# Kernel tuning notes

Measured on AMD Instinct MI355X. Metric: run time of the kernel, lower is better.

## Reference

```python
import jax, jax.numpy as jnp
import numpy as np

N = 1024
X_DIM = 128
Y_DIM = 128
HIDDEN = 256


def setup_inputs() -> dict:
    key = jax.random.key(0)
    ks = jax.random.split(key, 6)
    x_samples = jax.random.normal(ks[0], (N, X_DIM), dtype=jnp.float32)
    y_samples = jax.random.normal(ks[1], (N, Y_DIM), dtype=jnp.float32)
    in_dim = X_DIM + Y_DIM
    # Linear params (kaiming-uniform-ish small init)
    W1 = jax.random.normal(ks[2], (in_dim, HIDDEN), dtype=jnp.float32) / np.sqrt(in_dim)
    b1 = jnp.zeros((HIDDEN,), dtype=jnp.float32)
    W2 = jax.random.normal(ks[3], (HIDDEN, 1), dtype=jnp.float32) / np.sqrt(HIDDEN)
    b2 = jnp.zeros((1,), dtype=jnp.float32)
    return {"x_samples": x_samples, "y_samples": y_samples,
            "W1": W1, "b1": b1, "W2": W2, "b2": b2}


def reference(x_samples, y_samples, W1, b1, W2, b2):
    n = y_samples.shape[0]
    W1x, W1y = W1[:X_DIM], W1[X_DIM:]
    xp = x_samples @ W1x          # [N, H]  (x_tile[i, j] = x[j])
    yp = y_samples @ W1y          # [N, H]  (y_tile[i, j] = y[i])
    # T0: F(cat([x_i, y_i])) on the diagonal pairs -> [N, 1]
    T0 = jax.nn.relu(xp + yp + b1) @ W2 + b2
    # T1: F over all pairs (i, j) -> [N, N, 1]
    h = jax.nn.relu(yp[:, None, :] + xp[None, :, :] + b1)   # [N, N, H]
    T1 = h @ W2 + b2                                        # [N, N, 1]
    lse = jax.scipy.special.logsumexp(T1, axis=1)           # [N, 1] over dim=1
    lower_bound = T0.mean() - (lse.mean() - jnp.log(jnp.float32(n)))
    return lower_bound
```

## Files before the change

kernel.cpp:

```cpp
#include <hip/hip_runtime.h>

#define N_SAMP 1024
#define XD     128
#define HID    256


__global__ __launch_bounds__(256) void gemm_xy(
    const float* __restrict__ x, const float* __restrict__ y,
    const float* __restrict__ W1, const float* __restrict__ b1,
    float* __restrict__ xpbT, float* __restrict__ ypT,
    float* __restrict__ S, float* __restrict__ T0sum)
{
    const int k  = threadIdx.x;
    const int r0 = blockIdx.x * 4;

    if (threadIdx.x < 4) S[blockIdx.x * 4 + threadIdx.x] = 0.f;
    if (blockIdx.x == 0 && threadIdx.x == 4) T0sum[0] = 0.f;

    float ax0 = 0.f, ax1 = 0.f, ax2 = 0.f, ax3 = 0.f;
    float ay0 = 0.f, ay1 = 0.f, ay2 = 0.f, ay3 = 0.f;

    #pragma unroll 4
    for (int d = 0; d < XD; ++d) {
        const float wx = W1[d * HID + k];
        const float wy = W1[(XD + d) * HID + k];
        ax0 = fmaf(x[(r0 + 0) * XD + d], wx, ax0);
        ax1 = fmaf(x[(r0 + 1) * XD + d], wx, ax1);
        ax2 = fmaf(x[(r0 + 2) * XD + d], wx, ax2);
        ax3 = fmaf(x[(r0 + 3) * XD + d], wx, ax3);
        ay0 = fmaf(y[(r0 + 0) * XD + d], wy, ay0);
        ay1 = fmaf(y[(r0 + 1) * XD + d], wy, ay1);
        ay2 = fmaf(y[(r0 + 2) * XD + d], wy, ay2);
        ay3 = fmaf(y[(r0 + 3) * XD + d], wy, ay3);
    }

    const float bk = b1[k];
    float4 xs = make_float4(ax0 + bk, ax1 + bk, ax2 + bk, ax3 + bk);
    float4 ys = make_float4(ay0, ay1, ay2, ay3);
    *(float4*)&xpbT[k * N_SAMP + r0] = xs;
    *(float4*)&ypT [k * N_SAMP + r0] = ys;
}

__global__ __launch_bounds__(256) void pair_lse(
    const float* __restrict__ ypT, const float* __restrict__ xpbT,
    const float* __restrict__ W2,
    float* __restrict__ S, float* __restrict__ T0sum)
{
    const int tid = threadIdx.x;
    const int tj  = tid & 15;
    const int ti  = tid >> 4;
    const int bj  = blockIdx.x;
    const int bi  = blockIdx.y;
    const int j0  = bj * 64 + tj * 4;
    const int i0  = bi * 32 + ti * 2;

    float acc[2][4];
    #pragma unroll
    for (int a = 0; a < 2; ++a)
        #pragma unroll
        for (int b = 0; b < 4; ++b) acc[a][b] = 0.f;

    #pragma unroll 4
    for (int k = 0; k < HID; ++k) {
        const float4 xv = *(const float4*)&xpbT[k * N_SAMP + j0];
        const float2 yv = *(const float2*)&ypT [k * N_SAMP + i0];
        const float  w  = W2[k];
        acc[0][0] = fmaf(fmaxf(yv.x + xv.x, 0.f), w, acc[0][0]);
        acc[0][1] = fmaf(fmaxf(yv.x + xv.y, 0.f), w, acc[0][1]);
        acc[0][2] = fmaf(fmaxf(yv.x + xv.z, 0.f), w, acc[0][2]);
        acc[0][3] = fmaf(fmaxf(yv.x + xv.w, 0.f), w, acc[0][3]);
        acc[1][0] = fmaf(fmaxf(yv.y + xv.x, 0.f), w, acc[1][0]);
        acc[1][1] = fmaf(fmaxf(yv.y + xv.y, 0.f), w, acc[1][1]);
        acc[1][2] = fmaf(fmaxf(yv.y + xv.z, 0.f), w, acc[1][2]);
        acc[1][3] = fmaf(fmaxf(yv.y + xv.w, 0.f), w, acc[1][3]);
    }

    #pragma unroll
    for (int a = 0; a < 2; ++a) {
        float e = __expf(acc[a][0]) + __expf(acc[a][1])
                + __expf(acc[a][2]) + __expf(acc[a][3]);
        #pragma unroll
        for (int off = 8; off; off >>= 1) e += __shfl_xor(e, off, 16);
        if (tj == 0) atomicAdd(&S[i0 + a], e);
    }

    if (bj == (bi >> 1)) {
        float dv = 0.f;
        #pragma unroll
        for (int a = 0; a < 2; ++a)
            #pragma unroll
            for (int b = 0; b < 4; ++b)
                if (i0 + a == j0 + b) dv += acc[a][b];
        #pragma unroll
        for (int off = 32; off; off >>= 1) dv += __shfl_xor(dv, off, 64);
        if ((tid & 63) == 0) atomicAdd(T0sum, dv);
    }
}

__global__ __launch_bounds__(256) void finalize(
    const float* __restrict__ S, const float* __restrict__ T0sum,
    const float* __restrict__ b2, float* __restrict__ out)
{
    __shared__ float red[4];
    const int tid = threadIdx.x;

    float ls = 0.f;
    for (int i = tid; i < N_SAMP; i += 256) ls += logf(S[i]);
    #pragma unroll
    for (int off = 32; off; off >>= 1) ls += __shfl_xor(ls, off, 64);
    if ((tid & 63) == 0) red[tid >> 6] = ls;
    __syncthreads();

    if (tid == 0) {
        const float lse_sum = red[0] + red[1] + red[2] + red[3];
        const float t0_mean  = T0sum[0] / (float)N_SAMP + b2[0];
        const float lse_mean = lse_sum / (float)N_SAMP + b2[0] - logf((float)N_SAMP);
        out[0] = t0_mean - lse_mean;
    }
}

extern "C" void kernel_launch(void* const* d_in, const int* in_sizes, int n_in,
                              void* d_out, int out_size, void* d_ws, size_t ws_size,
                              hipStream_t stream)
{
    const float* x  = (const float*)d_in[0];
    const float* y  = (const float*)d_in[1];
    const float* W1 = (const float*)d_in[2];
    const float* b1 = (const float*)d_in[3];
    const float* W2 = (const float*)d_in[4];
    const float* b2 = (const float*)d_in[5];

    float* ws   = (float*)d_ws;
    float* S    = ws;
    float* T0s  = ws + 1024;
    float* xpbT = ws + 2048;
    float* ypT  = ws + 2048 + HID * N_SAMP;

    gemm_xy <<<dim3(N_SAMP / 4), dim3(256), 0, stream>>>(x, y, W1, b1,
                                                         xpbT, ypT, S, T0s);
    pair_lse<<<dim3(16, 32),     dim3(256), 0, stream>>>(ypT, xpbT, W2, S, T0s);
    finalize<<<dim3(1),          dim3(256), 0, stream>>>(S, T0s, b2, (float*)d_out);
}
```

Measured before the change: 114.4 us.

## Stage y tile in LDS and compute 4x4 pair outputs per thread

```diff
diff --git a/kernel.cpp b/kernel.cpp
--- a/kernel.cpp
+++ b/kernel.cpp
@@ -41,42 +41,55 @@
     *(float4*)&ypT [k * N_SAMP + r0] = ys;
 }
 
-__global__ __launch_bounds__(256) void pair_lse(
+__global__ __launch_bounds__(128) void pair_lse(
     const float* __restrict__ ypT, const float* __restrict__ xpbT,
     const float* __restrict__ W2,
     float* __restrict__ S, float* __restrict__ T0sum)
 {
+    __shared__ float yl[HID * 32];
+
     const int tid = threadIdx.x;
     const int tj  = tid & 15;
     const int ti  = tid >> 4;
-    const int bj  = blockIdx.x;
-    const int bi  = blockIdx.y;
-    const int j0  = bj * 64 + tj * 4;
-    const int i0  = bi * 32 + ti * 2;
+    const int jb  = blockIdx.x * 64;
+    const int ib  = blockIdx.y * 32;
+    const int j0  = jb + tj * 4;
+    const int i0  = ib + ti * 4;
 
-    float acc[2][4];
     #pragma unroll
-    for (int a = 0; a < 2; ++a)
+    for (int s = 0; s < 16; ++s) {
+        const int f  = s * 128 + tid;
+        const int k  = f >> 3;
+        const int iq = (f & 7) * 4;
+        *(float4*)&yl[k * 32 + iq] =
+            *(const float4*)&ypT[k * N_SAMP + ib + iq];
+    }
+    __syncthreads();
+
+    float acc[4][4];
+    #pragma unroll
+    for (int a = 0; a < 4; ++a)
         #pragma unroll
         for (int b = 0; b < 4; ++b) acc[a][b] = 0.f;
 
-    #pragma unroll 4
+    const int ti4 = ti * 4;
+
+    #pragma unroll 8
     for (int k = 0; k < HID; ++k) {
         const float4 xv = *(const float4*)&xpbT[k * N_SAMP + j0];
-        const float2 yv = *(const float2*)&ypT [k * N_SAMP + i0];
+        const float4 yv = *(const float4*)&yl[k * 32 + ti4];
         const float  w  = W2[k];
-        acc[0][0] = fmaf(fmaxf(yv.x + xv.x, 0.f), w, acc[0][0]);
-        acc[0][1] = fmaf(fmaxf(yv.x + xv.y, 0.f), w, acc[0][1]);
-        acc[0][2] = fmaf(fmaxf(yv.x + xv.z, 0.f), w, acc[0][2]);
-        acc[0][3] = fmaf(fmaxf(yv.x + xv.w, 0.f), w, acc[0][3]);
-        acc[1][0] = fmaf(fmaxf(yv.y + xv.x, 0.f), w, acc[1][0]);
-        acc[1][1] = fmaf(fmaxf(yv.y + xv.y, 0.f), w, acc[1][1]);
-        acc[1][2] = fmaf(fmaxf(yv.y + xv.z, 0.f), w, acc[1][2]);
-        acc[1][3] = fmaf(fmaxf(yv.y + xv.w, 0.f), w, acc[1][3]);
+        const float xs[4] = {xv.x, xv.y, xv.z, xv.w};
+        const float ys[4] = {yv.x, yv.y, yv.z, yv.w};
+        #pragma unroll
+        for (int a = 0; a < 4; ++a)
+            #pragma unroll
+            for (int b = 0; b < 4; ++b)
+                acc[a][b] = fmaf(fmaxf(ys[a] + xs[b], 0.f), w, acc[a][b]);
     }
 
     #pragma unroll
-    for (int a = 0; a < 2; ++a) {
+    for (int a = 0; a < 4; ++a) {
         float e = __expf(acc[a][0]) + __expf(acc[a][1])
                 + __expf(acc[a][2]) + __expf(acc[a][3]);
         #pragma unroll
@@ -84,13 +97,18 @@
         if (tj == 0) atomicAdd(&S[i0 + a], e);
     }
 
-    if (bj == (bi >> 1)) {
+    if ((int)blockIdx.x == (int)(blockIdx.y >> 1)) {
         float dv = 0.f;
         #pragma unroll
-        for (int a = 0; a < 2; ++a)
-            #pragma unroll
-            for (int b = 0; b < 4; ++b)
-                if (i0 + a == j0 + b) dv += acc[a][b];
+        for (int a = 0; a < 4; ++a) {
+            const int dd = i0 + a - j0;
+            float t = 0.f;
+            if      (dd == 0) t = acc[a][0];
+            else if (dd == 1) t = acc[a][1];
+            else if (dd == 2) t = acc[a][2];
+            else if (dd == 3) t = acc[a][3];
+            dv += t;
+        }
         #pragma unroll
         for (int off = 32; off; off >>= 1) dv += __shfl_xor(dv, off, 64);
         if ((tid & 63) == 0) atomicAdd(T0sum, dv);
@@ -138,6 +156,6 @@
 
     gemm_xy <<<dim3(N_SAMP / 4), dim3(256), 0, stream>>>(x, y, W1, b1,
                                                          xpbT, ypT, S, T0s);
-    pair_lse<<<dim3(16, 32),     dim3(256), 0, stream>>>(ypT, xpbT, W2, S, T0s);
+    pair_lse<<<dim3(16, 32),     dim3(128), 0, stream>>>(ypT, xpbT, W2, S, T0s);
     finalize<<<dim3(1),          dim3(256), 0, stream>>>(S, T0s, b2, (float*)d_out);
 }
```

After: 120.5 us. +5.3%, slower.
